# Kernel optimization log

Measured on AMD Instinct MI355X. Metric: run time of the kernel, lower is better.

The kernel has to match this reference:

```python
import jax, jax.numpy as jnp
import numpy as np

LOW_DIM, SKIP_DIM, OUT_DIM = 512, 256, 256
EPS_IDW = 1e-8
EPS_LN = 1e-5
K = 3


def setup_inputs() -> dict:
    key = jax.random.key(0)
    ks = jax.random.split(key, 10)
    B, N, S = 4, 8192, 2048
    xyz_hi = jax.random.uniform(ks[0], (B, N, 3), dtype=jnp.float32)
    xyz_lo = jax.random.uniform(ks[1], (B, S, 3), dtype=jnp.float32)
    feat_skip = jax.random.normal(ks[2], (B, N, SKIP_DIM), dtype=jnp.float32)
    feat_lo = jax.random.normal(ks[3], (B, S, LOW_DIM), dtype=jnp.float32)
    in_dim = LOW_DIM + SKIP_DIM
    W1 = jax.random.normal(ks[4], (in_dim, OUT_DIM), dtype=jnp.float32) / np.sqrt(in_dim)
    b1 = jnp.zeros((OUT_DIM,), dtype=jnp.float32)
    W2 = jax.random.normal(ks[5], (OUT_DIM, OUT_DIM), dtype=jnp.float32) / np.sqrt(OUT_DIM)
    b2 = jnp.zeros((OUT_DIM,), dtype=jnp.float32)
    gamma = jnp.ones((OUT_DIM,), dtype=jnp.float32)
    beta = jnp.zeros((OUT_DIM,), dtype=jnp.float32)
    return {"xyz_hi": xyz_hi, "xyz_lo": xyz_lo, "feat_skip": feat_skip,
            "feat_lo": feat_lo, "W1": W1, "b1": b1, "W2": W2, "b2": b2,
            "gamma": gamma, "beta": beta}


def _layer_norm(x, gamma, beta):
    mu = jnp.mean(x, axis=-1, keepdims=True)
    var = jnp.mean(jnp.square(x - mu), axis=-1, keepdims=True)
    return (x - mu) * jax.lax.rsqrt(var + EPS_LN) * gamma + beta


def reference(xyz_hi, xyz_lo, feat_skip, feat_lo, W1, b1, W2, b2, gamma, beta):
    B, N, _ = xyz_hi.shape
    _, S, _ = xyz_lo.shape
    if S == 1:
        interpolated = jnp.broadcast_to(feat_lo, (B, N, feat_lo.shape[-1]))
    else:
        # pairwise Euclidean distances: (B, N, S)
        d2 = (jnp.sum(xyz_hi ** 2, -1)[:, :, None]
              + jnp.sum(xyz_lo ** 2, -1)[:, None, :]
              - 2.0 * jnp.einsum('bnd,bsd->bns', xyz_hi, xyz_lo))
        dists = jnp.sqrt(jnp.maximum(d2, 0.0))
        # smallest-3 via top_k on negated distances
        neg_d, knn_idx = jax.lax.top_k(-dists, K)          # (B, N, 3)
        dk = -neg_d
        inv_d = 1.0 / (dk + EPS_IDW)
        weights = inv_d / jnp.sum(inv_d, axis=-1, keepdims=True)  # (B, N, 3)
        # gather neighbor features: (B, N, 3, low_dim)
        knn_feat = feat_lo[jnp.arange(B)[:, None, None], knn_idx]
        interpolated = jnp.einsum('bnk,bnkc->bnc', weights, knn_feat)
    fused = jnp.concatenate([feat_skip, interpolated], axis=-1)   # (B, N, skip+low)
    h = jax.nn.relu(fused @ W1 + b1)
    h = h @ W2 + b2
    return _layer_norm(h, gamma, beta)
```

## Files before the change

kernel.cpp:

```cpp
#include <hip/hip_runtime.h>
#include <stdint.h>

typedef unsigned short u16;
typedef __attribute__((ext_vector_type(8))) short short8;
typedef __attribute__((ext_vector_type(4))) float f32x4;

#define BB 4
#define NN 8192
#define SS 2048
#define MTOT 32768
#define CSKIP 256
#define CLO 512
#define CIN 768
#define COUT 256
#define QPB 32
#define PARTS 8

__device__ __forceinline__ u16 f2bf(float f) {
  unsigned u = __float_as_uint(f);
  u += 0x7fffu + ((u >> 16) & 1u);
  return (u16)(u >> 16);
}

__device__ __forceinline__ void gl_lds16(const void* g, void* l) {
  __builtin_amdgcn_global_load_lds(
      (const __attribute__((address_space(1))) void*)g,
      (__attribute__((address_space(3))) void*)l, 16, 0, 0);
}

__global__ __launch_bounds__(256) void wconv_kernel(const float* __restrict__ W1,
                                                    const float* __restrict__ W2,
                                                    u16* __restrict__ W1T,
                                                    u16* __restrict__ W2T) {
  int i = blockIdx.x * 256 + threadIdx.x;
  if (i < CIN * COUT) {
    int n = i / CIN, k = i - n * CIN;
    W1T[i] = f2bf(W1[(size_t)k * COUT + n]);
  } else if (i < CIN * COUT + COUT * COUT) {
    int j = i - CIN * COUT;
    int n = j >> 8, k = j & 255;
    W2T[j] = f2bf(W2[(size_t)k * COUT + n]);
  }
}

__global__ __launch_bounds__(256, 4) void knn_interp_kernel(
    const float* __restrict__ xyz_hi, const float* __restrict__ xyz_lo,
    const float* __restrict__ feat_skip, const float* __restrict__ feat_lo,
    u16* __restrict__ fused) {
  __shared__ float4 sxyz[SS];
  __shared__ float md[QPB][25];
  __shared__ int   mi[QPB][25];
  __shared__ float wq[QPB][3];
  __shared__ int   iq[QPB][3];

  int tid = threadIdx.x;
  int blk = blockIdx.x;
  int b = blk >> 8;
  const float* xl = xyz_lo + (size_t)b * SS * 3;
  for (int j = tid; j < SS; j += 256)
    sxyz[j] = make_float4(xl[j * 3 + 0], xl[j * 3 + 1], xl[j * 3 + 2], 0.f);
  __syncthreads();

  int q = tid >> 3, part = tid & 7;
  int qm = blk * QPB + q;
  float qx = xyz_hi[(size_t)qm * 3 + 0];
  float qy = xyz_hi[(size_t)qm * 3 + 1];
  float qz = xyz_hi[(size_t)qm * 3 + 2];

  float bd0 = 1e30f, bd1 = 1e30f, bd2 = 1e30f;
  int bi0 = -1, bi1 = -1, bi2 = -1;
#pragma unroll 4
  for (int i = 0; i < SS / PARTS; ++i) {
    int j = part + i * PARTS;
    float4 p = sxyz[j];
    float dx = p.x - qx, dy = p.y - qy, dz = p.z - qz;
    float d2 = fmaf(dx, dx, fmaf(dy, dy, dz * dz));
    if (d2 < bd2) {
      bd2 = d2; bi2 = j;
      if (bd2 < bd1) { float t = bd1; bd1 = bd2; bd2 = t; int ti = bi1; bi1 = bi2; bi2 = ti; }
      if (bd1 < bd0) { float t = bd0; bd0 = bd1; bd1 = t; int ti = bi0; bi0 = bi1; bi1 = ti; }
    }
  }
  md[q][part * 3 + 0] = bd0; mi[q][part * 3 + 0] = bi0;
  md[q][part * 3 + 1] = bd1; mi[q][part * 3 + 1] = bi1;
  md[q][part * 3 + 2] = bd2; mi[q][part * 3 + 2] = bi2;
  __syncthreads();

  if (tid < QPB) {
    int qq = tid;
    float fb0 = 1e30f, fb1 = 1e30f, fb2 = 1e30f;
    int fi0 = -1, fi1 = -1, fi2 = -1;
    for (int u = 0; u < PARTS * 3; ++u) {
      float d = md[qq][u]; int ix = mi[qq][u];
      if (d < fb2 || (d == fb2 && ix < fi2)) {
        fb2 = d; fi2 = ix;
        if (fb2 < fb1 || (fb2 == fb1 && fi2 < fi1)) {
          float t = fb1; fb1 = fb2; fb2 = t; int ti = fi1; fi1 = fi2; fi2 = ti;
        }
        if (fb1 < fb0 || (fb1 == fb0 && fi1 < fi0)) {
          float t = fb0; fb0 = fb1; fb1 = t; int ti = fi0; fi0 = fi1; fi1 = ti;
        }
      }
    }
    float d0 = sqrtf(fb0), d1 = sqrtf(fb1), d2f = sqrtf(fb2);
    float inv0 = 1.0f / (d0 + 1e-8f);
    float inv1 = 1.0f / (d1 + 1e-8f);
    float inv2 = 1.0f / (d2f + 1e-8f);
    float s = inv0 + inv1 + inv2;
    wq[qq][0] = inv0 / s; wq[qq][1] = inv1 / s; wq[qq][2] = inv2 / s;
    iq[qq][0] = fi0; iq[qq][1] = fi1; iq[qq][2] = fi2;
  }
  __syncthreads();

  int wid = tid >> 6, lane = tid & 63;
  for (int qq = wid * 8; qq < wid * 8 + 8; ++qq) {
    int qm2 = blk * QPB + qq;
    float w0 = wq[qq][0], w1 = wq[qq][1], w2 = wq[qq][2];
    const float* f0 = feat_lo + ((size_t)b * SS + iq[qq][0]) * CLO + lane * 8;
    const float* f1 = feat_lo + ((size_t)b * SS + iq[qq][1]) * CLO + lane * 8;
    const float* f2 = feat_lo + ((size_t)b * SS + iq[qq][2]) * CLO + lane * 8;
    float4 a0 = ((const float4*)f0)[0], a1 = ((const float4*)f0)[1];
    float4 c0 = ((const float4*)f1)[0], c1 = ((const float4*)f1)[1];
    float4 e0 = ((const float4*)f2)[0], e1 = ((const float4*)f2)[1];
    float av[8];
    av[0] = w0 * a0.x + w1 * c0.x + w2 * e0.x;
    av[1] = w0 * a0.y + w1 * c0.y + w2 * e0.y;
    av[2] = w0 * a0.z + w1 * c0.z + w2 * e0.z;
    av[3] = w0 * a0.w + w1 * c0.w + w2 * e0.w;
    av[4] = w0 * a1.x + w1 * c1.x + w2 * e1.x;
    av[5] = w0 * a1.y + w1 * c1.y + w2 * e1.y;
    av[6] = w0 * a1.z + w1 * c1.z + w2 * e1.z;
    av[7] = w0 * a1.w + w1 * c1.w + w2 * e1.w;
    u16 ph[8];
#pragma unroll
    for (int c = 0; c < 8; ++c) ph[c] = f2bf(av[c]);
    uint4 st; __builtin_memcpy(&st, ph, 16);
    *(uint4*)(fused + (size_t)qm2 * CIN + CSKIP + lane * 8) = st;

    float4 sk = *(const float4*)(feat_skip + (size_t)qm2 * CSKIP + lane * 4);
    u16 p4[4];
    p4[0] = f2bf(sk.x); p4[1] = f2bf(sk.y); p4[2] = f2bf(sk.z); p4[3] = f2bf(sk.w);
    uint2 st2; __builtin_memcpy(&st2, p4, 8);
    *(uint2*)(fused + (size_t)qm2 * CIN + lane * 4) = st2;
  }
}

__global__ __launch_bounds__(256) void gemm1_kernel(const u16* __restrict__ A,
                                                    const u16* __restrict__ Bt,
                                                    const float* __restrict__ b1,
                                                    u16* __restrict__ H) {
  __shared__ u16 As[128 * 32];
  __shared__ u16 Bs[128 * 32];
  int tid = threadIdx.x;
  int bm = blockIdx.x >> 1, bn = blockIdx.x & 1;
  int m0 = bm << 7, n0 = bn << 7;
  int w = tid >> 6, lane = tid & 63;
  int wr = w >> 1, wc = w & 1;
  int quad = lane >> 4, l16 = lane & 15;

  f32x4 zero = {0.f, 0.f, 0.f, 0.f};
  f32x4 acc[4][4];
#pragma unroll
  for (int tm = 0; tm < 4; ++tm)
#pragma unroll
    for (int tn = 0; tn < 4; ++tn) acc[tm][tn] = zero;

  for (int k0 = 0; k0 < CIN; k0 += 32) {
    __syncthreads();
#pragma unroll
    for (int r = 0; r < 2; ++r) {
      int u = tid + r * 256;
      int row = u >> 2, kk = (u & 3) << 3;
      gl_lds16(A + (size_t)(m0 + row) * CIN + k0 + kk, (char*)As + u * 16);
      gl_lds16(Bt + (size_t)(n0 + row) * CIN + k0 + kk, (char*)Bs + u * 16);
    }
    __syncthreads();
    short8 af[4], bf[4];
#pragma unroll
    for (int t = 0; t < 4; ++t)
      af[t] = *(const short8*)(As + ((wr * 64 + t * 16 + l16) * 32 + quad * 8));
#pragma unroll
    for (int t = 0; t < 4; ++t)
      bf[t] = *(const short8*)(Bs + ((wc * 64 + t * 16 + l16) * 32 + quad * 8));
#pragma unroll
    for (int tm = 0; tm < 4; ++tm)
#pragma unroll
      for (int tn = 0; tn < 4; ++tn)
        acc[tm][tn] = __builtin_amdgcn_mfma_f32_16x16x32_bf16(af[tm], bf[tn], acc[tm][tn], 0, 0, 0);
  }

  float bias[4];
#pragma unroll
  for (int tn = 0; tn < 4; ++tn) bias[tn] = b1[n0 + wc * 64 + tn * 16 + l16];
#pragma unroll
  for (int tm = 0; tm < 4; ++tm)
#pragma unroll
    for (int tn = 0; tn < 4; ++tn) {
      int col = n0 + wc * 64 + tn * 16 + l16;
#pragma unroll
      for (int r = 0; r < 4; ++r) {
        int row = m0 + wr * 64 + tm * 16 + quad * 4 + r;
        float v = acc[tm][tn][r] + bias[tn];
        v = v > 0.f ? v : 0.f;
        H[(size_t)row * COUT + col] = f2bf(v);
      }
    }
}

__global__ __launch_bounds__(512) void gemm2_ln_kernel(const u16* __restrict__ H,
                                                       const u16* __restrict__ Bt,
                                                       const float* __restrict__ b2,
                                                       const float* __restrict__ gamma,
                                                       const float* __restrict__ beta,
                                                       float* __restrict__ out) {
  __shared__ u16 As[128 * 32];
  __shared__ u16 Bs[256 * 32];
  __shared__ float red[4][128][2];
  __shared__ float stats[128][2];
  int tid = threadIdx.x;
  int m0 = blockIdx.x << 7;
  int w = tid >> 6, lane = tid & 63;
  int wr = w >> 2, wc = w & 3;
  int quad = lane >> 4, l16 = lane & 15;

  f32x4 zero = {0.f, 0.f, 0.f, 0.f};
  f32x4 acc[4][4];
#pragma unroll
  for (int tm = 0; tm < 4; ++tm)
#pragma unroll
    for (int tn = 0; tn < 4; ++tn) acc[tm][tn] = zero;

  for (int k0 = 0; k0 < COUT; k0 += 32) {
    __syncthreads();
    {
      int row = tid >> 2, kk = (tid & 3) << 3;
      gl_lds16(H + (size_t)(m0 + row) * COUT + k0 + kk, (char*)As + tid * 16);
#pragma unroll
      for (int r = 0; r < 2; ++r) {
        int ub = tid + r * 512;
        int nrow = ub >> 2, kb = (ub & 3) << 3;
        gl_lds16(Bt + (size_t)nrow * COUT + k0 + kb, (char*)Bs + ub * 16);
      }
    }
    __syncthreads();
    short8 af[4], bf[4];
#pragma unroll
    for (int t = 0; t < 4; ++t)
      af[t] = *(const short8*)(As + ((wr * 64 + t * 16 + l16) * 32 + quad * 8));
#pragma unroll
    for (int t = 0; t < 4; ++t)
      bf[t] = *(const short8*)(Bs + ((wc * 64 + t * 16 + l16) * 32 + quad * 8));
#pragma unroll
    for (int tm = 0; tm < 4; ++tm)
#pragma unroll
      for (int tn = 0; tn < 4; ++tn)
        acc[tm][tn] = __builtin_amdgcn_mfma_f32_16x16x32_bf16(af[tm], bf[tn], acc[tm][tn], 0, 0, 0);
  }

  float bias[4], g[4], be[4];
#pragma unroll
  for (int tn = 0; tn < 4; ++tn) {
    int col = wc * 64 + tn * 16 + l16;
    bias[tn] = b2[col]; g[tn] = gamma[col]; be[tn] = beta[col];
  }
#pragma unroll
  for (int tm = 0; tm < 4; ++tm)
#pragma unroll
    for (int r = 0; r < 4; ++r) {
      float s = 0.f, sq = 0.f;
#pragma unroll
      for (int tn = 0; tn < 4; ++tn) {
        float v = acc[tm][tn][r] + bias[tn];
        acc[tm][tn][r] = v;
        s += v; sq += v * v;
      }
#pragma unroll
      for (int msk = 1; msk < 16; msk <<= 1) {
        s += __shfl_xor(s, msk);
        sq += __shfl_xor(sq, msk);
      }
      if (l16 == 0) {
        int rl = wr * 64 + tm * 16 + quad * 4 + r;
        red[wc][rl][0] = s;
        red[wc][rl][1] = sq;
      }
    }
  __syncthreads();
  if (tid < 128) {
    float s = red[0][tid][0] + red[1][tid][0] + red[2][tid][0] + red[3][tid][0];
    float sq = red[0][tid][1] + red[1][tid][1] + red[2][tid][1] + red[3][tid][1];
    float mu = s * (1.f / 256.f);
    float var = sq * (1.f / 256.f) - mu * mu;
    stats[tid][0] = mu;
    stats[tid][1] = rsqrtf(var + 1e-5f);
  }
  __syncthreads();
#pragma unroll
  for (int tm = 0; tm < 4; ++tm)
#pragma unroll
    for (int r = 0; r < 4; ++r) {
      int rl = wr * 64 + tm * 16 + quad * 4 + r;
      float mu = stats[rl][0], rstd = stats[rl][1];
#pragma unroll
      for (int tn = 0; tn < 4; ++tn) {
        int col = wc * 64 + tn * 16 + l16;
        out[(size_t)(m0 + rl) * COUT + col] = (acc[tm][tn][r] - mu) * rstd * g[tn] + be[tn];
      }
    }
}

extern "C" void kernel_launch(void* const* d_in, const int* in_sizes, int n_in,
                              void* d_out, int out_size, void* d_ws, size_t ws_size,
                              hipStream_t stream) {
  const float* xyz_hi    = (const float*)d_in[0];
  const float* xyz_lo    = (const float*)d_in[1];
  const float* feat_skip = (const float*)d_in[2];
  const float* feat_lo   = (const float*)d_in[3];
  const float* W1        = (const float*)d_in[4];
  const float* b1        = (const float*)d_in[5];
  const float* W2        = (const float*)d_in[6];
  const float* b2        = (const float*)d_in[7];
  const float* gamma     = (const float*)d_in[8];
  const float* beta      = (const float*)d_in[9];
  float* out = (float*)d_out;

  char* ws = (char*)d_ws;
  u16* fused = (u16*)ws;
  u16* H     = (u16*)(ws + 50331648);
  u16* W1T   = (u16*)(ws + 50331648 + 16777216);
  u16* W2T   = (u16*)(ws + 50331648 + 16777216 + 393216);

  wconv_kernel<<<1024, 256, 0, stream>>>(W1, W2, W1T, W2T);
  knn_interp_kernel<<<MTOT / QPB, 256, 0, stream>>>(xyz_hi, xyz_lo, feat_skip, feat_lo, fused);
  gemm1_kernel<<<(MTOT / 128) * 2, 256, 0, stream>>>(fused, W1T, b1, H);
  gemm2_ln_kernel<<<MTOT / 128, 512, 0, stream>>>(H, W2T, b2, gamma, beta, out);
}
```

Baseline: 208.6 us.

## Fuse interpolation gather into GEMM1 A-tile load and split KNN into own kernel

The KNN kernel now writes only the neighbour weights and indices to global memory, and its per-query scan uses branchless selects with 8 waves each covering a contiguous slice of the low-res points. GEMM1 builds its A tile on the fly by reading feat_skip or gathering three feat_lo rows, blending them, and converting to bf16 into LDS. The full-width 256-column B tile uses 512 threads. This removes the 48 MB bf16 fused intermediate write and read-back. The cost is that the A-tile loads become synchronous register loads that are not overlapped with the MFMA work, and the gather reads three rows per output row.

```diff
diff --git a/kernel.cpp b/kernel.cpp
--- a/kernel.cpp
+++ b/kernel.cpp
@@ -1,4 +1,5 @@
 #include <hip/hip_runtime.h>
+#include <hip/hip_bf16.h>
 #include <stdint.h>
 
 typedef unsigned short u16;
@@ -13,8 +14,6 @@
 #define CLO 512
 #define CIN 768
 #define COUT 256
-#define QPB 32
-#define PARTS 8
 
 __device__ __forceinline__ u16 f2bf(float f) {
   unsigned u = __float_as_uint(f);
@@ -43,120 +42,110 @@
   }
 }
 
-__global__ __launch_bounds__(256, 4) void knn_interp_kernel(
+__global__ __launch_bounds__(512) void knn_kernel(
     const float* __restrict__ xyz_hi, const float* __restrict__ xyz_lo,
-    const float* __restrict__ feat_skip, const float* __restrict__ feat_lo,
-    u16* __restrict__ fused) {
+    float* __restrict__ wq_g, int* __restrict__ iq_g) {
   __shared__ float4 sxyz[SS];
-  __shared__ float md[QPB][25];
-  __shared__ int   mi[QPB][25];
-  __shared__ float wq[QPB][3];
-  __shared__ int   iq[QPB][3];
+  __shared__ float md[8][64][3];
+  __shared__ int   mi[8][64][3];
 
   int tid = threadIdx.x;
   int blk = blockIdx.x;
-  int b = blk >> 8;
+  int b = blk >> 7;
   const float* xl = xyz_lo + (size_t)b * SS * 3;
-  for (int j = tid; j < SS; j += 256)
+  for (int j = tid; j < SS; j += 512)
     sxyz[j] = make_float4(xl[j * 3 + 0], xl[j * 3 + 1], xl[j * 3 + 2], 0.f);
   __syncthreads();
 
-  int q = tid >> 3, part = tid & 7;
-  int qm = blk * QPB + q;
+  int wave = tid >> 6, lane = tid & 63;
+  int qm = blk * 64 + lane;
   float qx = xyz_hi[(size_t)qm * 3 + 0];
   float qy = xyz_hi[(size_t)qm * 3 + 1];
   float qz = xyz_hi[(size_t)qm * 3 + 2];
 
-  float bd0 = 1e30f, bd1 = 1e30f, bd2 = 1e30f;
-  int bi0 = -1, bi1 = -1, bi2 = -1;
+  float b0 = 1e30f, b1 = 1e30f, b2 = 1e30f;
+  int i0 = -1, i1 = -1, i2 = -1;
+  int j0 = wave * 256;
 #pragma unroll 4
-  for (int i = 0; i < SS / PARTS; ++i) {
-    int j = part + i * PARTS;
+  for (int jj = 0; jj < 256; ++jj) {
+    int j = j0 + jj;
     float4 p = sxyz[j];
     float dx = p.x - qx, dy = p.y - qy, dz = p.z - qz;
-    float d2 = fmaf(dx, dx, fmaf(dy, dy, dz * dz));
-    if (d2 < bd2) {
-      bd2 = d2; bi2 = j;
-      if (bd2 < bd1) { float t = bd1; bd1 = bd2; bd2 = t; int ti = bi1; bi1 = bi2; bi2 = ti; }
-      if (bd1 < bd0) { float t = bd0; bd0 = bd1; bd1 = t; int ti = bi0; bi0 = bi1; bi1 = ti; }
-    }
-  }
-  md[q][part * 3 + 0] = bd0; mi[q][part * 3 + 0] = bi0;
-  md[q][part * 3 + 1] = bd1; mi[q][part * 3 + 1] = bi1;
-  md[q][part * 3 + 2] = bd2; mi[q][part * 3 + 2] = bi2;
+    float d = fmaf(dx, dx, fmaf(dy, dy, dz * dz));
+    bool c = d < b2;
+    b2 = c ? d : b2; i2 = c ? j : i2;
+    bool s = b2 < b1;
+    float tb = b1; b1 = s ? b2 : b1; b2 = s ? tb : b2;
+    int ti = i1;   i1 = s ? i2 : i1; i2 = s ? ti : i2;
+    bool v = b1 < b0;
+    float ub = b0; b0 = v ? b1 : b0; b1 = v ? ub : b1;
+    int ui = i0;   i0 = v ? i1 : i0; i1 = v ? ui : i1;
+  }
+  md[wave][lane][0] = b0; mi[wave][lane][0] = i0;
+  md[wave][lane][1] = b1; mi[wave][lane][1] = i1;
+  md[wave][lane][2] = b2; mi[wave][lane][2] = i2;
   __syncthreads();
 
-  if (tid < QPB) {
-    int qq = tid;
+  if (tid < 64) {
+    int q = tid;
     float fb0 = 1e30f, fb1 = 1e30f, fb2 = 1e30f;
     int fi0 = -1, fi1 = -1, fi2 = -1;
-    for (int u = 0; u < PARTS * 3; ++u) {
-      float d = md[qq][u]; int ix = mi[qq][u];
-      if (d < fb2 || (d == fb2 && ix < fi2)) {
-        fb2 = d; fi2 = ix;
-        if (fb2 < fb1 || (fb2 == fb1 && fi2 < fi1)) {
-          float t = fb1; fb1 = fb2; fb2 = t; int ti = fi1; fi1 = fi2; fi2 = ti;
+    for (int p = 0; p < 8; ++p)
+#pragma unroll
+      for (int s = 0; s < 3; ++s) {
+        float d = md[p][q][s]; int ix = mi[p][q][s];
+        if (d < fb2 || (d == fb2 && ix < fi2)) {
+          fb2 = d; fi2 = ix;
+          if (fb2 < fb1 || (fb2 == fb1 && fi2 < fi1)) {
+            float t = fb1; fb1 = fb2; fb2 = t; int ti = fi1; fi1 = fi2; fi2 = ti;
+          }
+          if (fb1 < fb0 || (fb1 == fb0 && fi1 < fi0)) {
+            float t = fb0; fb0 = fb1; fb1 = t; int ti = fi0; fi0 = fi1; fi1 = ti;
+          }
         }
-        if (fb1 < fb0 || (fb1 == fb0 && fi1 < fi0)) {
-          float t = fb0; fb0 = fb1; fb1 = t; int ti = fi0; fi0 = fi1; fi1 = ti;
-        }
-      }
-    }
-    float d0 = sqrtf(fb0), d1 = sqrtf(fb1), d2f = sqrtf(fb2);
+      }
+    int qm2 = blk * 64 + q;
+    float d0 = sqrtf(fb0), d1 = sqrtf(fb1), d2 = sqrtf(fb2);
     float inv0 = 1.0f / (d0 + 1e-8f);
     float inv1 = 1.0f / (d1 + 1e-8f);
-    float inv2 = 1.0f / (d2f + 1e-8f);
+    float inv2 = 1.0f / (d2 + 1e-8f);
     float s = inv0 + inv1 + inv2;
-    wq[qq][0] = inv0 / s; wq[qq][1] = inv1 / s; wq[qq][2] = inv2 / s;
-    iq[qq][0] = fi0; iq[qq][1] = fi1; iq[qq][2] = fi2;
-  }
-  __syncthreads();
-
-  int wid = tid >> 6, lane = tid & 63;
-  for (int qq = wid * 8; qq < wid * 8 + 8; ++qq) {
-    int qm2 = blk * QPB + qq;
-    float w0 = wq[qq][0], w1 = wq[qq][1], w2 = wq[qq][2];
-    const float* f0 = feat_lo + ((size_t)b * SS + iq[qq][0]) * CLO + lane * 8;
-    const float* f1 = feat_lo + ((size_t)b * SS + iq[qq][1]) * CLO + lane * 8;
-    const float* f2 = feat_lo + ((size_t)b * SS + iq[qq][2]) * CLO + lane * 8;
-    float4 a0 = ((const float4*)f0)[0], a1 = ((const float4*)f0)[1];
-    float4 c0 = ((const float4*)f1)[0], c1 = ((const float4*)f1)[1];
-    float4 e0 = ((const float4*)f2)[0], e1 = ((const float4*)f2)[1];
-    float av[8];
-    av[0] = w0 * a0.x + w1 * c0.x + w2 * e0.x;
-    av[1] = w0 * a0.y + w1 * c0.y + w2 * e0.y;
-    av[2] = w0 * a0.z + w1 * c0.z + w2 * e0.z;
-    av[3] = w0 * a0.w + w1 * c0.w + w2 * e0.w;
-    av[4] = w0 * a1.x + w1 * c1.x + w2 * e1.x;
-    av[5] = w0 * a1.y + w1 * c1.y + w2 * e1.y;
-    av[6] = w0 * a1.z + w1 * c1.z + w2 * e1.z;
-    av[7] = w0 * a1.w + w1 * c1.w + w2 * e1.w;
-    u16 ph[8];
-#pragma unroll
-    for (int c = 0; c < 8; ++c) ph[c] = f2bf(av[c]);
-    uint4 st; __builtin_memcpy(&st, ph, 16);
-    *(uint4*)(fused + (size_t)qm2 * CIN + CSKIP + lane * 8) = st;
-
-    float4 sk = *(const float4*)(feat_skip + (size_t)qm2 * CSKIP + lane * 4);
-    u16 p4[4];
-    p4[0] = f2bf(sk.x); p4[1] = f2bf(sk.y); p4[2] = f2bf(sk.z); p4[3] = f2bf(sk.w);
-    uint2 st2; __builtin_memcpy(&st2, p4, 8);
-    *(uint2*)(fused + (size_t)qm2 * CIN + lane * 4) = st2;
-  }
-}
-
-__global__ __launch_bounds__(256) void gemm1_kernel(const u16* __restrict__ A,
-                                                    const u16* __restrict__ Bt,
-                                                    const float* __restrict__ b1,
-                                                    u16* __restrict__ H) {
+    wq_g[(size_t)qm2 * 3 + 0] = inv0 / s;
+    wq_g[(size_t)qm2 * 3 + 1] = inv1 / s;
+    wq_g[(size_t)qm2 * 3 + 2] = inv2 / s;
+    iq_g[(size_t)qm2 * 3 + 0] = fi0;
+    iq_g[(size_t)qm2 * 3 + 1] = fi1;
+    iq_g[(size_t)qm2 * 3 + 2] = fi2;
+  }
+}
+
+__global__ __launch_bounds__(512) void gemm1_fused_kernel(
+    const float* __restrict__ feat_skip, const float* __restrict__ feat_lo,
+    const float* __restrict__ wq_g, const int* __restrict__ iq_g,
+    const u16* __restrict__ W1T, const float* __restrict__ b1,
+    u16* __restrict__ H) {
   __shared__ u16 As[128 * 32];
-  __shared__ u16 Bs[128 * 32];
+  __shared__ u16 Bs[256 * 32];
   int tid = threadIdx.x;
-  int bm = blockIdx.x >> 1, bn = blockIdx.x & 1;
-  int m0 = bm << 7, n0 = bn << 7;
+  int m0 = blockIdx.x << 7;
+  int b = blockIdx.x >> 6;
   int w = tid >> 6, lane = tid & 63;
-  int wr = w >> 1, wc = w & 1;
+  int wr = w >> 2, wc = w & 3;
   int quad = lane >> 4, l16 = lane & 15;
+
+  int srow = tid >> 2;
+  int sc8 = (tid & 3) << 3;
+  float w0 = wq_g[(size_t)(m0 + srow) * 3 + 0];
+  float w1 = wq_g[(size_t)(m0 + srow) * 3 + 1];
+  float w2 = wq_g[(size_t)(m0 + srow) * 3 + 2];
+  int i0 = iq_g[(size_t)(m0 + srow) * 3 + 0];
+  int i1 = iq_g[(size_t)(m0 + srow) * 3 + 1];
+  int i2 = iq_g[(size_t)(m0 + srow) * 3 + 2];
+  const float* fl0 = feat_lo + ((size_t)b * SS + i0) * CLO + sc8;
+  const float* fl1 = feat_lo + ((size_t)b * SS + i1) * CLO + sc8;
+  const float* fl2 = feat_lo + ((size_t)b * SS + i2) * CLO + sc8;
+  const float* fsk = feat_skip + (size_t)(m0 + srow) * CSKIP + sc8;
+  u16* As_dst = As + srow * 32 + sc8;
 
   f32x4 zero = {0.f, 0.f, 0.f, 0.f};
   f32x4 acc[4][4];
@@ -165,16 +154,41 @@
 #pragma unroll
     for (int tn = 0; tn < 4; ++tn) acc[tm][tn] = zero;
 
-  for (int k0 = 0; k0 < CIN; k0 += 32) {
+  for (int kc = 0; kc < 24; ++kc) {
     __syncthreads();
 #pragma unroll
     for (int r = 0; r < 2; ++r) {
-      int u = tid + r * 256;
-      int row = u >> 2, kk = (u & 3) << 3;
-      gl_lds16(A + (size_t)(m0 + row) * CIN + k0 + kk, (char*)As + u * 16);
-      gl_lds16(Bt + (size_t)(n0 + row) * CIN + k0 + kk, (char*)Bs + u * 16);
-    }
+      int u = tid + r * 512;
+      int nrow = u >> 2, kb = (u & 3) << 3;
+      gl_lds16(W1T + (size_t)nrow * CIN + kc * 32 + kb, (char*)Bs + u * 16);
+    }
+    float av[8];
+    if (kc < 8) {
+      float4 x0 = *(const float4*)(fsk + kc * 32);
+      float4 x1 = *(const float4*)(fsk + kc * 32 + 4);
+      av[0] = x0.x; av[1] = x0.y; av[2] = x0.z; av[3] = x0.w;
+      av[4] = x1.x; av[5] = x1.y; av[6] = x1.z; av[7] = x1.w;
+    } else {
+      int c = (kc - 8) * 32;
+      float4 a0 = *(const float4*)(fl0 + c), a1 = *(const float4*)(fl0 + c + 4);
+      float4 c0 = *(const float4*)(fl1 + c), c1 = *(const float4*)(fl1 + c + 4);
+      float4 e0 = *(const float4*)(fl2 + c), e1 = *(const float4*)(fl2 + c + 4);
+      av[0] = fmaf(w0, a0.x, fmaf(w1, c0.x, w2 * e0.x));
+      av[1] = fmaf(w0, a0.y, fmaf(w1, c0.y, w2 * e0.y));
+      av[2] = fmaf(w0, a0.z, fmaf(w1, c0.z, w2 * e0.z));
+      av[3] = fmaf(w0, a0.w, fmaf(w1, c0.w, w2 * e0.w));
+      av[4] = fmaf(w0, a1.x, fmaf(w1, c1.x, w2 * e1.x));
+      av[5] = fmaf(w0, a1.y, fmaf(w1, c1.y, w2 * e1.y));
+      av[6] = fmaf(w0, a1.z, fmaf(w1, c1.z, w2 * e1.z));
+      av[7] = fmaf(w0, a1.w, fmaf(w1, c1.w, w2 * e1.w));
+    }
+    union { __hip_bfloat162 h2[4]; uint4 u4; } pk;
+#pragma unroll
+    for (int c = 0; c < 4; ++c)
+      pk.h2[c] = __float22bfloat162_rn(make_float2(av[2 * c], av[2 * c + 1]));
+    *(uint4*)As_dst = pk.u4;
     __syncthreads();
+
     short8 af[4], bf[4];
 #pragma unroll
     for (int t = 0; t < 4; ++t)
@@ -191,12 +205,12 @@
 
   float bias[4];
 #pragma unroll
-  for (int tn = 0; tn < 4; ++tn) bias[tn] = b1[n0 + wc * 64 + tn * 16 + l16];
+  for (int tn = 0; tn < 4; ++tn) bias[tn] = b1[wc * 64 + tn * 16 + l16];
 #pragma unroll
   for (int tm = 0; tm < 4; ++tm)
 #pragma unroll
     for (int tn = 0; tn < 4; ++tn) {
-      int col = n0 + wc * 64 + tn * 16 + l16;
+      int col = wc * 64 + tn * 16 + l16;
 #pragma unroll
       for (int r = 0; r < 4; ++r) {
         int row = m0 + wr * 64 + tm * 16 + quad * 4 + r;
@@ -325,13 +339,14 @@
   float* out = (float*)d_out;
 
   char* ws = (char*)d_ws;
-  u16* fused = (u16*)ws;
-  u16* H     = (u16*)(ws + 50331648);
-  u16* W1T   = (u16*)(ws + 50331648 + 16777216);
-  u16* W2T   = (u16*)(ws + 50331648 + 16777216 + 393216);
+  u16*   H    = (u16*)ws;
+  u16*   W1T  = (u16*)(ws + 16777216);
+  u16*   W2T  = (u16*)(ws + 16777216 + 393216);
+  float* wq_g = (float*)(ws + 16777216 + 393216 + 131072);
+  int*   iq_g = (int*)(ws + 16777216 + 393216 + 131072 + 393216);
 
   wconv_kernel<<<1024, 256, 0, stream>>>(W1, W2, W1T, W2T);
-  knn_interp_kernel<<<MTOT / QPB, 256, 0, stream>>>(xyz_hi, xyz_lo, feat_skip, feat_lo, fused);
-  gemm1_kernel<<<(MTOT / 128) * 2, 256, 0, stream>>>(fused, W1T, b1, H);
+  knn_kernel<<<MTOT / 64, 512, 0, stream>>>(xyz_hi, xyz_lo, wq_g, iq_g);
+  gemm1_fused_kernel<<<MTOT / 128, 512, 0, stream>>>(feat_skip, feat_lo, wq_g, iq_g, W1T, b1, H);
   gemm2_ln_kernel<<<MTOT / 128, 512, 0, stream>>>(H, W2T, b2, gamma, beta, out);
 }
```

Measured after the change: 197.4 us. -5.4%, faster.
